# Kernel tuning notes

Hardware: AMD Instinct MI355X
Metric: run time of the kernel (lower is better)

## Reference

```python
import jax, jax.numpy as jnp
import numpy as np

SCALE = 2
EPS = 1e-5  # BatchNorm2d default eps


def conv1x1(x, W, b):
    # x: [B,C,H,W], W: [O,C], b: [O]
    return jnp.einsum('bchw,oc->bohw', x, W) + b[None, :, None, None]


def maxpool(x, s):
    B, C, H, W = x.shape
    return x.reshape(B, C, H // s, s, W // s, s).max(axis=(3, 5))


def upsample_bilinear_ac(x, s):
    # bilinear upsample, align_corners=True
    B, C, H, W = x.shape
    Ho, Wo = H * s, W * s
    ys = jnp.arange(Ho) * ((H - 1) / (Ho - 1))
    xs = jnp.arange(Wo) * ((W - 1) / (Wo - 1))
    y0 = jnp.floor(ys).astype(jnp.int32)
    y1 = jnp.minimum(y0 + 1, H - 1)
    wy = (ys - y0).astype(x.dtype)
    x0 = jnp.floor(xs).astype(jnp.int32)
    x1 = jnp.minimum(x0 + 1, W - 1)
    wx = (xs - x0).astype(x.dtype)
    rows = x[:, :, y0, :] * (1 - wy)[None, None, :, None] + x[:, :, y1, :] * wy[None, None, :, None]
    return rows[:, :, :, x0] * (1 - wx) + rows[:, :, :, x1] * wx


def setup_inputs() -> dict:
    key = jax.random.key(0)
    ks = jax.random.split(key, 9)
    B, Cin, Cm, dk, H, W = 4, 64, 64, 64, 128, 128
    return {
        'x': jax.random.normal(ks[0], (B, Cin, H, W), jnp.float32),
        'memory': jax.random.normal(ks[1], (B, Cm, H, W), jnp.float32),
        'W_qkv': jax.random.normal(ks[2], (3 * dk, Cm), jnp.float32) * 0.05,
        'b_qkv': jax.random.normal(ks[3], (3 * dk,), jnp.float32) * 0.05,
        'W_out': jax.random.normal(ks[4], (Cin, dk), jnp.float32) * 0.05,
        'b_out': jax.random.normal(ks[5], (Cin,), jnp.float32) * 0.05,
        'bn_gamma': jax.random.uniform(ks[6], (Cin,), jnp.float32, 0.5, 1.5),
        'bn_beta': jax.random.normal(ks[7], (Cin,), jnp.float32) * 0.05,
        'gamma': jax.random.normal(ks[8], (1,), jnp.float32) * 0.1,
    }


def reference(x, memory, W_qkv, b_qkv, W_out, b_out, bn_gamma, bn_beta, gamma):
    d_k = W_qkv.shape[0] // 3
    qkv = conv1x1(memory, W_qkv, b_qkv)
    qkv = maxpool(qkv, SCALE)
    q, k, v = jnp.split(qkv, 3, axis=1)
    B, C, H, W = v.shape
    q = q.reshape(B, C, H * W).transpose(0, 2, 1)  # [B,N,C]
    k = k.reshape(B, C, H * W)                      # [B,C,N]
    v = v.reshape(B, C, H * W).transpose(0, 2, 1)   # [B,N,C]
    scale = jnp.asarray(d_k, x.dtype) ** 0.5
    attn = jax.nn.softmax(jnp.einsum('bnc,bcm->bnm', q, k) / scale, axis=-1)
    S = jnp.einsum('bnm,bmc->bnc', attn, v).transpose(0, 2, 1).reshape(B, C, H, W)
    S = upsample_bilinear_ac(S, SCALE)
    S = conv1x1(S, W_out, b_out)
    # BatchNorm2d (training mode: biased batch stats over B,H,W)
    mean = S.mean(axis=(0, 2, 3), keepdims=True)
    var = S.var(axis=(0, 2, 3), keepdims=True)
    S = (S - mean) / jnp.sqrt(var + EPS) * bn_gamma[None, :, None, None] + bn_beta[None, :, None, None]
    return x + gamma[0] * S
```

## Files before the change

### kernel.cpp

```cpp
#include <hip/hip_runtime.h>
#include <stdint.h>

typedef unsigned short u16;
typedef unsigned int   u32;
typedef __attribute__((ext_vector_type(8))) __bf16 bf16x8;
typedef __attribute__((ext_vector_type(4))) float  f32x4;
typedef __attribute__((ext_vector_type(2))) float  f32x2;
typedef __attribute__((ext_vector_type(4))) u32    u32x4;
typedef __attribute__((ext_vector_type(2))) u32    u32x2;

#define QSCALE 0.18033688011112042f

__device__ __forceinline__ u16 f2bf(float x) {
  u32 u = __builtin_bit_cast(u32, x);
  u = (u + 0x7FFFu + ((u >> 16) & 1u)) >> 16;
  return (u16)u;
}

__device__ __forceinline__ u32 cvt_pk_bf16(float lo, float hi) {
  u32 r;
  asm("v_cvt_pk_bf16_f32 %0, %1, %2" : "=v"(r) : "v"(lo), "v"(hi));
  return r;
}

__device__ __forceinline__ void gld16(const u16* g, u16* l) {
  __builtin_amdgcn_global_load_lds(
      (const __attribute__((address_space(1))) void*)g,
      (__attribute__((address_space(3))) void*)l, 16, 0, 0);
}

__global__ __launch_bounds__(512) void k_qkvpool(
    const float* __restrict__ mem, const float* __restrict__ Wqkv,
    const float* __restrict__ bqkv, const float* __restrict__ Wout,
    u16* __restrict__ Q, u16* __restrict__ K, u16* __restrict__ V,
    float* __restrict__ stats)
{
  const int oy = blockIdx.x, b = blockIdx.y, t = threadIdx.x;
  const int w = t >> 6, l4 = t & 15, lh = (t >> 4) & 3;
  const int wq = w & 3, wp = w >> 2;

  if (oy == 0 && b == 0 && t < 128) stats[t] = 0.f;

  __shared__ __align__(16) u16 lds[49152];
  u16* mlds  = lds;
  u16* wlds  = lds + 16384;
  u16* qlds  = lds + 28672;
  u16* klds  = lds + 32768;
  u16* vldsT = lds + 36864;
  u16* wolds = lds + 40960;
  u16* vplds = lds + 45056;

  float bias[3][4];
  #pragma unroll
  for (int j = 0; j < 3; ++j)
    #pragma unroll
    for (int r = 0; r < 4; ++r) {
      int oc = wq * 48 + 16 * j + lh * 4 + r;
      float bv = bqkv[oc];
      bias[j][r] = (oc < 64) ? bv * QSCALE : bv;
    }

  {
    const float* src = mem + ((size_t)b * 64) * 16384 + 2 * oy * 128;
    #pragma unroll
    for (int i = 0; i < 8; ++i) {
      int g = t + 512 * i;
      int px = g & 255, c0 = (g >> 8) * 4;
      float f0 = src[(size_t)(c0 + 0) * 16384 + px];
      float f1 = src[(size_t)(c0 + 1) * 16384 + px];
      float f2 = src[(size_t)(c0 + 2) * 16384 + px];
      float f3 = src[(size_t)(c0 + 3) * 16384 + px];
      u32x2 pk;
      pk[0] = (u32)f2bf(f0) | ((u32)f2bf(f1) << 16);
      pk[1] = (u32)f2bf(f2) | ((u32)f2bf(f3) << 16);
      *(u32x2*)(mlds + px * 64 + (((c0 * 2) ^ ((px & 7) << 4)) >> 1)) = pk;
    }
  }
  {
    #pragma unroll
    for (int i = 0; i < 6; ++i) {
      int g = t + 512 * i;
      int oc = g >> 4, c0 = (g & 15) * 4;
      f32x4 wv = *(const f32x4*)(Wqkv + oc * 64 + c0);
      u32x2 pk;
      pk[0] = (u32)f2bf(wv[0]) | ((u32)f2bf(wv[1]) << 16);
      pk[1] = (u32)f2bf(wv[2]) | ((u32)f2bf(wv[3]) << 16);
      *(u32x2*)(wlds + oc * 64 + (((c0 * 2) ^ ((oc & 7) << 4)) >> 1)) = pk;
    }
  }
  {
    #pragma unroll
    for (int i = 0; i < 2; ++i) {
      int g = t + 512 * i;
      int oc = g >> 4, c0 = (g & 15) * 4;
      f32x4 wv = *(const f32x4*)(Wout + oc * 64 + c0);
      u32x2 pk;
      pk[0] = (u32)f2bf(wv[0]) | ((u32)f2bf(wv[1]) << 16);
      pk[1] = (u32)f2bf(wv[2]) | ((u32)f2bf(wv[3]) << 16);
      *(u32x2*)(wolds + oc * 64 + (((c0 * 2) ^ ((oc & 7) << 4)) >> 1)) = pk;
    }
  }
  __syncthreads();

  const int sw  = (l4 & 7) << 4;
  const int oF0 = ((lh * 16) ^ sw) >> 1;
  const int oF1 = ((64 + lh * 16) ^ sw) >> 1;
  bf16x8 af[3][2];
  #pragma unroll
  for (int j = 0; j < 3; ++j) {
    const u16* ar = wlds + (wq * 48 + 16 * j + l4) * 64;
    af[j][0] = *(const bf16x8*)(ar + oF0);
    af[j][1] = *(const bf16x8*)(ar + oF1);
  }

  #pragma unroll 2
  for (int tpi = 0; tpi < 4; ++tpi) {
    const int tp = wp * 4 + tpi;
    const u16* br0 = mlds + (16 * tp + l4) * 64;
    const u16* br1 = mlds + (128 + 16 * tp + l4) * 64;
    bf16x8 b00 = *(const bf16x8*)(br0 + oF0);
    bf16x8 b01 = *(const bf16x8*)(br0 + oF1);
    bf16x8 b10 = *(const bf16x8*)(br1 + oF0);
    bf16x8 b11 = *(const bf16x8*)(br1 + oF1);
    const int ox = 8 * tp + (l4 >> 1);
    #pragma unroll
    for (int j = 0; j < 3; ++j) {
      f32x4 a0 = {0, 0, 0, 0}, a1 = {0, 0, 0, 0};
      a0 = __builtin_amdgcn_mfma_f32_16x16x32_bf16(af[j][0], b00, a0, 0, 0, 0);
      a0 = __builtin_amdgcn_mfma_f32_16x16x32_bf16(af[j][1], b01, a0, 0, 0, 0);
      a1 = __builtin_amdgcn_mfma_f32_16x16x32_bf16(af[j][0], b10, a1, 0, 0, 0);
      a1 = __builtin_amdgcn_mfma_f32_16x16x32_bf16(af[j][1], b11, a1, 0, 0, 0);
      const int ocj = wq * 48 + 16 * j;
      const float sc = (ocj < 64) ? QSCALE : 1.0f;
      #pragma unroll
      for (int r = 0; r < 4; ++r) {
        float m = fmaxf(a0[r], a1[r]);
        m = fmaxf(m, __shfl_xor(m, 1, 64));
        u16 val = f2bf(m * sc + bias[j][r]);
        if ((l4 & 1) == 0) {
          int oc = ocj + lh * 4 + r;
          if (ocj < 64)       qlds[ox * 64 + oc]        = val;
          else if (ocj < 128) klds[ox * 64 + (oc - 64)] = val;
          else {
            int vch = oc - 128;
            vldsT[ox * 64 + (((vch * 2) ^ ((ox & 7) << 4)) >> 1)] = val;
          }
        }
      }
    }
  }
  __syncthreads();

  {
    const u16* ar = wolds + (wq * 16 + l4) * 64;
    bf16x8 aw0 = *(const bf16x8*)(ar + oF0);
    bf16x8 aw1 = *(const bf16x8*)(ar + oF1);
    #pragma unroll
    for (int nti = 0; nti < 2; ++nti) {
      const int nt = wp * 2 + nti;
      const u16* brow = vldsT + (nt * 16 + l4) * 64;
      bf16x8 bw0 = *(const bf16x8*)(brow + oF0);
      bf16x8 bw1 = *(const bf16x8*)(brow + oF1);
      f32x4 u = {0, 0, 0, 0};
      u = __builtin_amdgcn_mfma_f32_16x16x32_bf16(aw0, bw0, u, 0, 0, 0);
      u = __builtin_amdgcn_mfma_f32_16x16x32_bf16(aw1, bw1, u, 0, 0, 0);
      #pragma unroll
      for (int r = 0; r < 4; ++r) {
        int oc = wq * 16 + lh * 4 + r;
        vplds[oc * 64 + nt * 16 + l4] = f2bf(u[r]);
      }
    }
  }
  __syncthreads();

  {
    int r = t >> 3, e8 = (t & 7) * 8;
    size_t nb = (size_t)oy * 64;
    *(u32x4*)(Q + ((size_t)b * 4096 + nb + r) * 64 + e8) = *(const u32x4*)(qlds + r * 64 + e8);
    int fbK = (r & 3) | (((r >> 3) & 1) << 2);
    int ksw = ((e8 * 2) ^ (fbK << 4)) >> 1;
    *(u32x4*)(K + ((size_t)b * 64 + oy) * 4096 + r * 64 + ksw) = *(const u32x4*)(klds + r * 64 + e8);
    int vsw2 = ((e8 * 2) ^ ((r & 7) << 4)) >> 1;
    *(u32x4*)(V + ((size_t)b * 64 + oy) * 4096 + r * 64 + vsw2) = *(const u32x4*)(vplds + r * 64 + e8);
  }
}

__global__ __launch_bounds__(1024, 4) void k_attn(
    const u16* __restrict__ Q, const u16* __restrict__ K,
    const u16* __restrict__ V, const float* __restrict__ bo,
    float* __restrict__ Sa)
{
  const int qb = blockIdx.x, b = blockIdx.y, t = threadIdx.x;
  const int w = t >> 6, l4 = t & 15, lh = (t >> 4) & 3;
  const int lane = t & 63;
  const int sgrp = w >> 2, wq = w & 3;

  __shared__ __align__(16) u16 kvbuf[65536];

  const int kofs = sgrp * 4096 + wq * 1024;
  const int vofs = 16384 + sgrp * 4096 + wq * 1024;
  const u16* kimg = K + ((size_t)b * 64 + sgrp * 16) * 4096 + wq * 1024 + lane * 8;
  const u16* vimg = V + ((size_t)b * 64 + sgrp * 16) * 4096 + wq * 1024 + lane * 8;

#define STAGE(BUF, KTI) {                                                     \
    const u16* kg = kimg + (size_t)(KTI) * 4096;                              \
    const u16* vg = vimg + (size_t)(KTI) * 4096;                              \
    gld16(kg,       (BUF) + kofs);                                            \
    gld16(kg + 512, (BUF) + kofs + 512);                                      \
    gld16(vg,       (BUF) + vofs);                                            \
    gld16(vg + 512, (BUF) + vofs + 512);                                      \
  }

  const int qrow = qb * 64 + wq * 16 + l4;
  const u16* qp = Q + ((size_t)b * 4096 + qrow) * 64 + lh * 8;
  bf16x8 qa0 = *(const bf16x8*)qp;
  bf16x8 qa1 = *(const bf16x8*)(qp + 32);

  f32x4 ot[4] = {{0,0,0,0},{0,0,0,0},{0,0,0,0},{0,0,0,0}};
  float lr = 0.f;

  const int rbase = ((l4 >> 2) << 3) + (l4 & 3);
  const int fbr   = ((l4 & 3) | (((l4 >> 2) & 1) << 2)) << 4;
  const int offL  = ((lh * 16) ^ fbr) >> 1;
  const int offH  = offL ^ 32;

#define ATTN_COMPUTE(BB)                                                      \
    _Pragma("unroll")                                                         \
    for (int ss = 0; ss < 2; ++ss) {                                          \
      const u16* kbase = (BB) + sgrp * 4096 + (ss * 32 + rbase) * 64;         \
      const u16* vbase = (BB) + 16384 + sgrp * 4096;                          \
      const int vswz = (((ss * 64 + lh * 16) ^ ((l4 & 7) << 4)) >> 1);        \
      bf16x8 vf0 = *(const bf16x8*)(vbase + (l4)      * 64 + vswz);           \
      bf16x8 vf1 = *(const bf16x8*)(vbase + (16 + l4) * 64 + vswz);           \
      bf16x8 vf2 = *(const bf16x8*)(vbase + (32 + l4) * 64 + vswz);           \
      bf16x8 vf3 = *(const bf16x8*)(vbase + (48 + l4) * 64 + vswz);           \
      bf16x8 k00 = *(const bf16x8*)(kbase + offL);                            \
      bf16x8 k01 = *(const bf16x8*)(kbase + offH);                            \
      bf16x8 k10 = *(const bf16x8*)(kbase + 256 + offL);                      \
      bf16x8 k11 = *(const bf16x8*)(kbase + 256 + offH);                      \
      f32x4 s0 = {0, 0, 0, 0}, s1 = {0, 0, 0, 0};                             \
      s0 = __builtin_amdgcn_mfma_f32_16x16x32_bf16(k00, qa0, s0, 0, 0, 0);    \
      s0 = __builtin_amdgcn_mfma_f32_16x16x32_bf16(k01, qa1, s0, 0, 0, 0);    \
      s1 = __builtin_amdgcn_mfma_f32_16x16x32_bf16(k10, qa0, s1, 0, 0, 0);    \
      s1 = __builtin_amdgcn_mfma_f32_16x16x32_bf16(k11, qa1, s1, 0, 0, 0);    \
      float p0[4], p1[4];                                                     \
      _Pragma("unroll")                                                       \
      for (int r = 0; r < 4; ++r) {                                           \
        p0[r] = exp2f(s0[r]);                                                 \
        p1[r] = exp2f(s1[r]);                                                 \
        lr += p0[r] + p1[r];                                                  \
      }                                                                       \
      u32x4 pw;                                                               \
      pw[0] = cvt_pk_bf16(p0[0], p0[1]);                                      \
      pw[1] = cvt_pk_bf16(p0[2], p0[3]);                                      \
      pw[2] = cvt_pk_bf16(p1[0], p1[1]);                                      \
      pw[3] = cvt_pk_bf16(p1[2], p1[3]);                                      \
      bf16x8 pf = __builtin_bit_cast(bf16x8, pw);                             \
      ot[0] = __builtin_amdgcn_mfma_f32_16x16x32_bf16(vf0, pf, ot[0], 0, 0, 0);\
      ot[1] = __builtin_amdgcn_mfma_f32_16x16x32_bf16(vf1, pf, ot[1], 0, 0, 0);\
      ot[2] = __builtin_amdgcn_mfma_f32_16x16x32_bf16(vf2, pf, ot[2], 0, 0, 0);\
      ot[3] = __builtin_amdgcn_mfma_f32_16x16x32_bf16(vf3, pf, ot[3], 0, 0, 0);\
    }

  STAGE(kvbuf, 0)

  #pragma unroll 1
  for (int kti = 0; kti < 16; ++kti) {
    u16* bufc = kvbuf + (kti & 1) * 32768;
    __syncthreads();
    if (kti < 15) STAGE(kvbuf + ((kti + 1) & 1) * 32768, kti + 1)
    ATTN_COMPUTE(bufc)
  }
  __syncthreads();
#undef ATTN_COMPUTE
#undef STAGE

  lr += __shfl_xor(lr, 16, 64);
  lr += __shfl_xor(lr, 32, 64);

  float* opb = (float*)kvbuf;
  float* mlb = (float*)(kvbuf + 32768);
  #pragma unroll
  for (int d = 0; d < 4; ++d)
    #pragma unroll
    for (int r = 0; r < 4; ++r)
      opb[w * 1024 + (16 * d + lh * 4 + r) * 16 + l4] = ot[d][r];
  if (lh == 0) mlb[w * 16 + l4] = lr;
  __syncthreads();

  const int ch = t >> 4, q0v = (t & 15) * 4;
  const float bout_c = bo[ch];
  f32x4 res;
  #pragma unroll
  for (int j = 0; j < 4; ++j) {
    int q = q0v + j, wq2 = q >> 4, ql = q & 15;
    float L = mlb[(wq2)*16      + ql] + mlb[(4 + wq2)*16  + ql]
            + mlb[(8 + wq2)*16  + ql] + mlb[(12 + wq2)*16 + ql];
    float O = opb[(wq2)*1024      + ch * 16 + ql]
            + opb[(4 + wq2)*1024  + ch * 16 + ql]
            + opb[(8 + wq2)*1024  + ch * 16 + ql]
            + opb[(12 + wq2)*1024 + ch * 16 + ql];
    res[j] = O / L + bout_c;
  }
  *(f32x4*)(Sa + ((size_t)b * 64 + ch) * 4096 + (size_t)qb * 64 + q0v) = res;
}

__global__ __launch_bounds__(1024) void k_stats(const float* __restrict__ U,
                                                float* __restrict__ stats)
{
  const int c = blockIdx.x & 63, b = blockIdx.x >> 6, t = threadIdx.x;
  __shared__ __align__(16) float up[4096];
  __shared__ float red[32];
  *(f32x4*)&up[t * 4] = *(const f32x4*)(U + ((size_t)b * 64 + c) * 4096 + t * 4);
  __syncthreads();
  const float R = 0.49606299212598425f;
  float sum = 0.f, ssq = 0.f;
  #pragma unroll
  for (int i = 0; i < 4; ++i) {
    const int px0 = i * 4096 + t * 4;
    const int yo = px0 >> 7, xo0 = px0 & 127;
    float ys = yo * R; int y0 = (int)ys; float wy = ys - y0;
    int y1 = min(y0 + 1, 63);
    const float* r0 = up + y0 * 64; const float* r1 = up + y1 * 64;
    #pragma unroll
    for (int j = 0; j < 4; ++j) {
      int xo = xo0 + j;
      float xs = xo * R; int x0 = (int)xs; float wx = xs - x0;
      int x1 = min(x0 + 1, 63);
      float v0 = r0[x0] * (1.f - wx) + r0[x1] * wx;
      float v1 = r1[x0] * (1.f - wx) + r1[x1] * wx;
      float v = v0 * (1.f - wy) + v1 * wy;
      sum += v; ssq += v * v;
    }
  }
  #pragma unroll
  for (int d = 32; d >= 1; d >>= 1) {
    sum += __shfl_down(sum, d, 64);
    ssq += __shfl_down(ssq, d, 64);
  }
  if ((t & 63) == 0) { red[t >> 6] = sum; red[16 + (t >> 6)] = ssq; }
  __syncthreads();
  if (t == 0) {
    float s = 0.f, q = 0.f;
    #pragma unroll
    for (int i = 0; i < 16; ++i) { s += red[i]; q += red[16 + i]; }
    atomicAdd(&stats[c], s);
    atomicAdd(&stats[64 + c], q);
  }
}

__global__ __launch_bounds__(1024) void k_apply(
    const float* __restrict__ U, const float* __restrict__ stats,
    const float* __restrict__ x, const float* __restrict__ bng,
    const float* __restrict__ bnb, const float* __restrict__ gam,
    float* __restrict__ out)
{
  const int c = blockIdx.x & 63, b = blockIdx.x >> 6, t = threadIdx.x;
  __shared__ __align__(16) float up[4096];
  *(f32x4*)&up[t * 4] = *(const f32x4*)(U + ((size_t)b * 64 + c) * 4096 + t * 4);
  __syncthreads();
  const float inv = 1.0f / 65536.0f;
  float mean = stats[c] * inv;
  float var  = stats[64 + c] * inv - mean * mean;
  float rsig = rsqrtf(var + 1e-5f);
  float g = gam[0];
  float A  = g * bng[c] * rsig;
  float Bc = g * (bnb[c] - mean * rsig * bng[c]);
  const float R = 0.49606299212598425f;
  const size_t base = ((size_t)b * 64 + c) * 16384;
  #pragma unroll
  for (int i = 0; i < 4; ++i) {
    const int px0 = i * 4096 + t * 4;
    const int yo = px0 >> 7, xo0 = px0 & 127;
    float ys = yo * R; int y0 = (int)ys; float wy = ys - y0;
    int y1 = min(y0 + 1, 63);
    const float* r0 = up + y0 * 64; const float* r1 = up + y1 * 64;
    f32x4 xv = *(const f32x4*)(x + base + px0);
    f32x4 ov;
    #pragma unroll
    for (int j = 0; j < 4; ++j) {
      int xo = xo0 + j;
      float xs = xo * R; int x0 = (int)xs; float wx = xs - x0;
      int x1 = min(x0 + 1, 63);
      float v0 = r0[x0] * (1.f - wx) + r0[x1] * wx;
      float v1 = r1[x0] * (1.f - wx) + r1[x1] * wx;
      float v = v0 * (1.f - wy) + v1 * wy;
      ov[j] = xv[j] + v * A + Bc;
    }
    *(f32x4*)(out + base + px0) = ov;
  }
}

extern "C" void kernel_launch(void* const* d_in, const int* in_sizes, int n_in,
                              void* d_out, int out_size, void* d_ws, size_t ws_size,
                              hipStream_t stream)
{
  const float* x      = (const float*)d_in[0];
  const float* memory = (const float*)d_in[1];
  const float* Wqkv   = (const float*)d_in[2];
  const float* bqkv   = (const float*)d_in[3];
  const float* Wout   = (const float*)d_in[4];
  const float* bout   = (const float*)d_in[5];
  const float* bng    = (const float*)d_in[6];
  const float* bnb    = (const float*)d_in[7];
  const float* gamma  = (const float*)d_in[8];

  char* ws = (char*)d_ws;
  u16*   Q     = (u16*)(ws + 0);
  u16*   Kk    = (u16*)(ws + (2u << 20));
  u16*   Vt    = (u16*)(ws + (4u << 20));
  float* U     = (float*)(ws + (10u << 20));
  float* stats = (float*)(ws + (14u << 20));
  float* out   = (float*)d_out;

  k_qkvpool<<<dim3(64, 4), 512, 0, stream>>>(memory, Wqkv, bqkv, Wout, Q, Kk, Vt, stats);
  k_attn   <<<dim3(64, 4), 1024, 0, stream>>>(Q, Kk, Vt, bout, U);
  k_stats  <<<256, 1024, 0, stream>>>(U, stats);
  k_apply  <<<256, 1024, 0, stream>>>(U, stats, x, bng, bnb, gamma, out);
}
```

Baseline: 61.17 us.

## Repartition attention waves to share K/V fragments across two query sub-tiles

Each wave now holds two 16-row query tiles (A and B) and handles only one of the two 32-key halves per staged tile, rather than one query tile over both halves. K and V fragments read from LDS are reused by both query tiles, which halves LDS fragment reads per MFMA and exposes more independent MFMA chains. The cost is more accumulator registers per wave, which is risky at 1024 threads per block. The final cross-wave reduction buffer is enlarged, so the shared array grows slightly, and the reduction switches to vectorized f32x4 reads over eight partial waves.

```diff
diff --git a/kernel.cpp b/kernel.cpp
--- a/kernel.cpp
+++ b/kernel.cpp
@@ -193,9 +193,12 @@
   const int qb = blockIdx.x, b = blockIdx.y, t = threadIdx.x;
   const int w = t >> 6, l4 = t & 15, lh = (t >> 4) & 3;
   const int lane = t & 63;
-  const int sgrp = w >> 2, wq = w & 3;
-
-  __shared__ __align__(16) u16 kvbuf[65536];
+  const int sgrp = w >> 2;
+  const int wq = w & 3;
+  const int qh = (w >> 1) & 1;
+  const int ssw = w & 1;
+
+  __shared__ __align__(16) u16 kvbuf[66560];
 
   const int kofs = sgrp * 4096 + wq * 1024;
   const int vofs = 16384 + sgrp * 4096 + wq * 1024;
@@ -211,56 +214,22 @@
     gld16(vg + 512, (BUF) + vofs + 512);                                      \
   }
 
-  const int qrow = qb * 64 + wq * 16 + l4;
-  const u16* qp = Q + ((size_t)b * 4096 + qrow) * 64 + lh * 8;
-  bf16x8 qa0 = *(const bf16x8*)qp;
-  bf16x8 qa1 = *(const bf16x8*)(qp + 32);
-
-  f32x4 ot[4] = {{0,0,0,0},{0,0,0,0},{0,0,0,0},{0,0,0,0}};
-  float lr = 0.f;
+  const int qrowA = qb * 64 + qh * 32 + l4;
+  const u16* qpA = Q + ((size_t)b * 4096 + qrowA) * 64 + lh * 8;
+  bf16x8 qaA0 = *(const bf16x8*)qpA;
+  bf16x8 qaA1 = *(const bf16x8*)(qpA + 32);
+  bf16x8 qaB0 = *(const bf16x8*)(qpA + 16 * 64);
+  bf16x8 qaB1 = *(const bf16x8*)(qpA + 16 * 64 + 32);
+
+  f32x4 otA0 = {0,0,0,0}, otA1 = {0,0,0,0}, otA2 = {0,0,0,0}, otA3 = {0,0,0,0};
+  f32x4 otB0 = {0,0,0,0}, otB1 = {0,0,0,0}, otB2 = {0,0,0,0}, otB3 = {0,0,0,0};
+  float lrA = 0.f, lrB = 0.f;
 
   const int rbase = ((l4 >> 2) << 3) + (l4 & 3);
   const int fbr   = ((l4 & 3) | (((l4 >> 2) & 1) << 2)) << 4;
   const int offL  = ((lh * 16) ^ fbr) >> 1;
   const int offH  = offL ^ 32;
-
-#define ATTN_COMPUTE(BB)                                                      \
-    _Pragma("unroll")                                                         \
-    for (int ss = 0; ss < 2; ++ss) {                                          \
-      const u16* kbase = (BB) + sgrp * 4096 + (ss * 32 + rbase) * 64;         \
-      const u16* vbase = (BB) + 16384 + sgrp * 4096;                          \
-      const int vswz = (((ss * 64 + lh * 16) ^ ((l4 & 7) << 4)) >> 1);        \
-      bf16x8 vf0 = *(const bf16x8*)(vbase + (l4)      * 64 + vswz);           \
-      bf16x8 vf1 = *(const bf16x8*)(vbase + (16 + l4) * 64 + vswz);           \
-      bf16x8 vf2 = *(const bf16x8*)(vbase + (32 + l4) * 64 + vswz);           \
-      bf16x8 vf3 = *(const bf16x8*)(vbase + (48 + l4) * 64 + vswz);           \
-      bf16x8 k00 = *(const bf16x8*)(kbase + offL);                            \
-      bf16x8 k01 = *(const bf16x8*)(kbase + offH);                            \
-      bf16x8 k10 = *(const bf16x8*)(kbase + 256 + offL);                      \
-      bf16x8 k11 = *(const bf16x8*)(kbase + 256 + offH);                      \
-      f32x4 s0 = {0, 0, 0, 0}, s1 = {0, 0, 0, 0};                             \
-      s0 = __builtin_amdgcn_mfma_f32_16x16x32_bf16(k00, qa0, s0, 0, 0, 0);    \
-      s0 = __builtin_amdgcn_mfma_f32_16x16x32_bf16(k01, qa1, s0, 0, 0, 0);    \
-      s1 = __builtin_amdgcn_mfma_f32_16x16x32_bf16(k10, qa0, s1, 0, 0, 0);    \
-      s1 = __builtin_amdgcn_mfma_f32_16x16x32_bf16(k11, qa1, s1, 0, 0, 0);    \
-      float p0[4], p1[4];                                                     \
-      _Pragma("unroll")                                                       \
-      for (int r = 0; r < 4; ++r) {                                           \
-        p0[r] = exp2f(s0[r]);                                                 \
-        p1[r] = exp2f(s1[r]);                                                 \
-        lr += p0[r] + p1[r];                                                  \
-      }                                                                       \
-      u32x4 pw;                                                               \
-      pw[0] = cvt_pk_bf16(p0[0], p0[1]);                                      \
-      pw[1] = cvt_pk_bf16(p0[2], p0[3]);                                      \
-      pw[2] = cvt_pk_bf16(p1[0], p1[1]);                                      \
-      pw[3] = cvt_pk_bf16(p1[2], p1[3]);                                      \
-      bf16x8 pf = __builtin_bit_cast(bf16x8, pw);                             \
-      ot[0] = __builtin_amdgcn_mfma_f32_16x16x32_bf16(vf0, pf, ot[0], 0, 0, 0);\
-      ot[1] = __builtin_amdgcn_mfma_f32_16x16x32_bf16(vf1, pf, ot[1], 0, 0, 0);\
-      ot[2] = __builtin_amdgcn_mfma_f32_16x16x32_bf16(vf2, pf, ot[2], 0, 0, 0);\
-      ot[3] = __builtin_amdgcn_mfma_f32_16x16x32_bf16(vf3, pf, ot[3], 0, 0, 0);\
-    }
+  const int vswz  = ((ssw * 64 + lh * 16) ^ ((l4 & 7) << 4)) >> 1;
 
   STAGE(kvbuf, 0)
 
@@ -269,40 +238,101 @@
     u16* bufc = kvbuf + (kti & 1) * 32768;
     __syncthreads();
     if (kti < 15) STAGE(kvbuf + ((kti + 1) & 1) * 32768, kti + 1)
-    ATTN_COMPUTE(bufc)
-  }
-  __syncthreads();
-#undef ATTN_COMPUTE
+
+    const u16* kbase = bufc + sgrp * 4096 + (ssw * 32 + rbase) * 64;
+    const u16* vbase = bufc + 16384 + sgrp * 4096;
+    bf16x8 vf0 = *(const bf16x8*)(vbase + (l4)      * 64 + vswz);
+    bf16x8 vf1 = *(const bf16x8*)(vbase + (16 + l4) * 64 + vswz);
+    bf16x8 vf2 = *(const bf16x8*)(vbase + (32 + l4) * 64 + vswz);
+    bf16x8 vf3 = *(const bf16x8*)(vbase + (48 + l4) * 64 + vswz);
+    bf16x8 k00 = *(const bf16x8*)(kbase + offL);
+    bf16x8 k01 = *(const bf16x8*)(kbase + offH);
+    bf16x8 k10 = *(const bf16x8*)(kbase + 256 + offL);
+    bf16x8 k11 = *(const bf16x8*)(kbase + 256 + offH);
+
+    f32x4 s0A = {0,0,0,0}, s1A = {0,0,0,0}, s0B = {0,0,0,0}, s1B = {0,0,0,0};
+    s0A = __builtin_amdgcn_mfma_f32_16x16x32_bf16(k00, qaA0, s0A, 0, 0, 0);
+    s0A = __builtin_amdgcn_mfma_f32_16x16x32_bf16(k01, qaA1, s0A, 0, 0, 0);
+    s1A = __builtin_amdgcn_mfma_f32_16x16x32_bf16(k10, qaA0, s1A, 0, 0, 0);
+    s1A = __builtin_amdgcn_mfma_f32_16x16x32_bf16(k11, qaA1, s1A, 0, 0, 0);
+    s0B = __builtin_amdgcn_mfma_f32_16x16x32_bf16(k00, qaB0, s0B, 0, 0, 0);
+    s0B = __builtin_amdgcn_mfma_f32_16x16x32_bf16(k01, qaB1, s0B, 0, 0, 0);
+    s1B = __builtin_amdgcn_mfma_f32_16x16x32_bf16(k10, qaB0, s1B, 0, 0, 0);
+    s1B = __builtin_amdgcn_mfma_f32_16x16x32_bf16(k11, qaB1, s1B, 0, 0, 0);
+
+    float pA0[4], pA1[4], pB0[4], pB1[4];
+    #pragma unroll
+    for (int r = 0; r < 4; ++r) {
+      pA0[r] = exp2f(s0A[r]);  pA1[r] = exp2f(s1A[r]);
+      pB0[r] = exp2f(s0B[r]);  pB1[r] = exp2f(s1B[r]);
+      lrA += pA0[r] + pA1[r];
+      lrB += pB0[r] + pB1[r];
+    }
+    u32x4 pwA, pwB;
+    pwA[0] = cvt_pk_bf16(pA0[0], pA0[1]);
+    pwA[1] = cvt_pk_bf16(pA0[2], pA0[3]);
+    pwA[2] = cvt_pk_bf16(pA1[0], pA1[1]);
+    pwA[3] = cvt_pk_bf16(pA1[2], pA1[3]);
+    pwB[0] = cvt_pk_bf16(pB0[0], pB0[1]);
+    pwB[1] = cvt_pk_bf16(pB0[2], pB0[3]);
+    pwB[2] = cvt_pk_bf16(pB1[0], pB1[1]);
+    pwB[3] = cvt_pk_bf16(pB1[2], pB1[3]);
+    bf16x8 pfA = __builtin_bit_cast(bf16x8, pwA);
+    bf16x8 pfB = __builtin_bit_cast(bf16x8, pwB);
+
+    otA0 = __builtin_amdgcn_mfma_f32_16x16x32_bf16(vf0, pfA, otA0, 0, 0, 0);
+    otA1 = __builtin_amdgcn_mfma_f32_16x16x32_bf16(vf1, pfA, otA1, 0, 0, 0);
+    otA2 = __builtin_amdgcn_mfma_f32_16x16x32_bf16(vf2, pfA, otA2, 0, 0, 0);
+    otA3 = __builtin_amdgcn_mfma_f32_16x16x32_bf16(vf3, pfA, otA3, 0, 0, 0);
+    otB0 = __builtin_amdgcn_mfma_f32_16x16x32_bf16(vf0, pfB, otB0, 0, 0, 0);
+    otB1 = __builtin_amdgcn_mfma_f32_16x16x32_bf16(vf1, pfB, otB1, 0, 0, 0);
+    otB2 = __builtin_amdgcn_mfma_f32_16x16x32_bf16(vf2, pfB, otB2, 0, 0, 0);
+    otB3 = __builtin_amdgcn_mfma_f32_16x16x32_bf16(vf3, pfB, otB3, 0, 0, 0);
+  }
+  __syncthreads();
 #undef STAGE
 
-  lr += __shfl_xor(lr, 16, 64);
-  lr += __shfl_xor(lr, 32, 64);
+  lrA += __shfl_xor(lrA, 16, 64);
+  lrA += __shfl_xor(lrA, 32, 64);
+  lrB += __shfl_xor(lrB, 16, 64);
+  lrB += __shfl_xor(lrB, 32, 64);
 
   float* opb = (float*)kvbuf;
-  float* mlb = (float*)(kvbuf + 32768);
-  #pragma unroll
-  for (int d = 0; d < 4; ++d)
-    #pragma unroll
-    for (int r = 0; r < 4; ++r)
-      opb[w * 1024 + (16 * d + lh * 4 + r) * 16 + l4] = ot[d][r];
-  if (lh == 0) mlb[w * 16 + l4] = lr;
-  __syncthreads();
-
-  const int ch = t >> 4, q0v = (t & 15) * 4;
+  float* mlb = ((float*)kvbuf) + 32768;
+  #pragma unroll
+  for (int d = 0; d < 4; ++d) {
+    f32x4 oa = d == 0 ? otA0 : (d == 1 ? otA1 : (d == 2 ? otA2 : otA3));
+    f32x4 ob = d == 0 ? otB0 : (d == 1 ? otB1 : (d == 2 ? otB2 : otB3));
+    #pragma unroll
+    for (int r = 0; r < 4; ++r) {
+      opb[w * 2048 + (16 * d + lh * 4 + r) * 32 + l4]      = oa[r];
+      opb[w * 2048 + (16 * d + lh * 4 + r) * 32 + 16 + l4] = ob[r];
+    }
+  }
+  if (lh == 0) {
+    mlb[w * 32 + l4]      = lrA;
+    mlb[w * 32 + 16 + l4] = lrB;
+  }
+  __syncthreads();
+
+  const int ch = t >> 4, q0 = (t & 15) * 4;
+  const int mqh = q0 >> 5, ql = q0 & 31;
   const float bout_c = bo[ch];
+  f32x4 Osum = {0, 0, 0, 0}, Lsum = {0, 0, 0, 0};
+  #pragma unroll
+  for (int s = 0; s < 4; ++s)
+    #pragma unroll
+    for (int e = 0; e < 2; ++e) {
+      const int pw_ = 4 * s + 2 * mqh + e;
+      f32x4 Ov = *(const f32x4*)&opb[pw_ * 2048 + ch * 32 + ql];
+      f32x4 Lv = *(const f32x4*)&mlb[pw_ * 32 + ql];
+      #pragma unroll
+      for (int j = 0; j < 4; ++j) { Osum[j] += Ov[j]; Lsum[j] += Lv[j]; }
+    }
   f32x4 res;
   #pragma unroll
-  for (int j = 0; j < 4; ++j) {
-    int q = q0v + j, wq2 = q >> 4, ql = q & 15;
-    float L = mlb[(wq2)*16      + ql] + mlb[(4 + wq2)*16  + ql]
-            + mlb[(8 + wq2)*16  + ql] + mlb[(12 + wq2)*16 + ql];
-    float O = opb[(wq2)*1024      + ch * 16 + ql]
-            + opb[(4 + wq2)*1024  + ch * 16 + ql]
-            + opb[(8 + wq2)*1024  + ch * 16 + ql]
-            + opb[(12 + wq2)*1024 + ch * 16 + ql];
-    res[j] = O / L + bout_c;
-  }
-  *(f32x4*)(Sa + ((size_t)b * 64 + ch) * 4096 + (size_t)qb * 64 + q0v) = res;
+  for (int j = 0; j < 4; ++j) res[j] = Osum[j] / Lsum[j] + bout_c;
+  *(f32x4*)(Sa + ((size_t)b * 64 + ch) * 4096 + (size_t)qb * 64 + q0) = res;
 }
 
 __global__ __launch_bounds__(1024) void k_stats(const float* __restrict__ U,
```

Result: no change. 62.19 us (+1.7%).
